# Kernel tuning notes

Hardware: AMD Instinct MI355X
Metric: run time of the kernel (lower is better)

Reference implementation:

```python
import jax, jax.numpy as jnp
import numpy as np

N_NODES = 50000


def setup_inputs() -> dict:
    key = jax.random.key(0)
    k1, k2, k3, k4, k5, k6 = jax.random.split(key, 6)
    c_in, c_out = 64, 64
    n_edges = 800000
    G = jax.random.normal(k1, (N_NODES, c_in), dtype=jnp.float32)
    RSC = jax.random.normal(k2, (N_NODES, c_in), dtype=jnp.float32)
    src = jax.random.randint(k3, (n_edges,), 0, N_NODES, dtype=jnp.int64)
    dst = jax.random.randint(k4, (n_edges,), 0, N_NODES, dtype=jnp.int64)
    W = jax.random.normal(k5, (c_out, c_in), dtype=jnp.float32) / np.sqrt(c_in)
    b = jax.random.normal(k6, (c_out,), dtype=jnp.float32) * 0.01
    return {"G": G, "RSC": RSC, "src": src, "dst": dst, "W": W, "b": b}


def reference(G, RSC, src, dst, W, b):
    # Per-edge relative feature: src node 'G' feature minus dst node 'RSC' feature
    rel = G[src] - RSC[dst]                          # [E, c_in]
    # Linear + ReLU (edge MLP)
    enc = jax.nn.relu(rel @ W.T + b)                 # [E, c_out]
    # Per-dst-node reductions over variable-size mailboxes
    max_agg = jax.ops.segment_max(enc, dst, num_segments=N_NODES)  # -inf for empty
    sum_agg = jax.ops.segment_sum(enc, dst, num_segments=N_NODES)
    cnt = jax.ops.segment_sum(jnp.ones_like(dst, dtype=enc.dtype), dst,
                              num_segments=N_NODES)               # [N]
    has_mail = (cnt > 0)[:, None]
    avg_agg = sum_agg / jnp.maximum(cnt, 1.0)[:, None]
    max_agg = jnp.where(has_mail, max_agg, 0.0)      # nodes w/o edges -> 0
    # concat(max, avg) as in reduce()
    return jnp.concatenate([max_agg, avg_agg], axis=-1)  # [N, 2*c_out]
```

## Files before the change

kernel.cpp:

```cpp
#include <hip/hip_runtime.h>
#include <hip/hip_bf16.h>

#define NCH 64
#define SPAN 64
#define HIST_BLOCKS 256
#define HIST_THREADS 1024
#define NBIN 256
#define NGEMM 768
#define FUSE_THREADS 512
#define SORT_CAP 3072

__global__ void detect_init_kernel(const unsigned short* __restrict__ gp, int n16,
                                   const unsigned* __restrict__ ip, int niw,
                                   unsigned* __restrict__ flags,
                                   unsigned* __restrict__ gcnt, int nb) {
    if (blockIdx.x == 0) {
        __shared__ unsigned se, so;
        if (threadIdx.x == 0) { se = 0u; so = 0u; }
        __syncthreads();
        unsigned le = 0u, lo = 0u;
        for (int i = threadIdx.x; i < n16; i += blockDim.x) {
            unsigned ex = (unsigned)((gp[i] >> 7) & 0xFFu);
            if (ex >= 0xC0u) le++;
        }
        for (int i = threadIdx.x; i < niw; i += blockDim.x) {
            if ((i & 1) && ip[i] != 0u) lo++;
        }
        atomicAdd(&se, le);
        atomicAdd(&so, lo);
        __syncthreads();
        if (threadIdx.x == 0) {
            flags[0] = (se > 50u) ? 1u : 0u;
            flags[1] = (so < 50u) ? 1u : 0u;
        }
    } else {
        const int stride = (gridDim.x - 1) * blockDim.x;
        for (int i = (blockIdx.x - 1) * blockDim.x + threadIdx.x; i < nb; i += stride)
            gcnt[i] = 0u;
    }
}

__global__ void bucket_hist_kernel(const void* __restrict__ dstp,
                                   unsigned* __restrict__ gcnt,
                                   const unsigned* __restrict__ flags,
                                   int n_edges, int nb) {
    extern __shared__ unsigned lcnt[];
    for (int i = threadIdx.x; i < nb; i += blockDim.x) lcnt[i] = 0u;
    __syncthreads();
    const unsigned i64 = flags[1];
    const int stride = gridDim.x * blockDim.x;
    for (int e = blockIdx.x * blockDim.x + threadIdx.x; e < n_edges; e += stride) {
        int d = i64 ? (int)((const long long*)dstp)[e] : ((const int*)dstp)[e];
        atomicAdd(&lcnt[d >> 6], 1u);
    }
    __syncthreads();
    for (int i = threadIdx.x; i < nb; i += blockDim.x)
        if (lcnt[i]) atomicAdd(&gcnt[i], lcnt[i]);
}

__global__ void bucket_scan_kernel(const unsigned* __restrict__ gcnt,
                                   unsigned* __restrict__ boffs,
                                   unsigned* __restrict__ cursor, int nb) {
    __shared__ unsigned s[1024];
    const int t = threadIdx.x;
    const int L = (nb + 1023) / 1024;
    unsigned local = 0u;
    for (int i = 0; i < L; ++i) {
        int idx = t * L + i;
        if (idx < nb) local += gcnt[idx];
    }
    s[t] = local;
    __syncthreads();
    for (int off = 1; off < 1024; off <<= 1) {
        unsigned v = (t >= off) ? s[t - off] : 0u;
        __syncthreads();
        s[t] += v;
        __syncthreads();
    }
    unsigned run = s[t] - local;
    for (int i = 0; i < L; ++i) {
        int idx = t * L + i;
        if (idx < nb) { boffs[idx] = run; cursor[idx] = run; run += gcnt[idx]; }
    }
}

__global__ __launch_bounds__(FUSE_THREADS, 4)
void binning_gemm_kernel(const void* __restrict__ srcp, const void* __restrict__ dstp,
                         unsigned* __restrict__ cursor, unsigned* __restrict__ binned,
                         const unsigned* __restrict__ flags, int n_edges, int nb,
                         int depth,
                         const void* __restrict__ Gp, const void* __restrict__ Rp,
                         const void* __restrict__ Wp, const void* __restrict__ bp,
                         void* __restrict__ PQ, int n_nodes) {
    extern __shared__ unsigned lds[];
    if (blockIdx.x < NBIN) {
        unsigned* lcnt = lds;
        unsigned* stage = lds + nb;
        for (int i = threadIdx.x; i < nb; i += blockDim.x) lcnt[i] = 0u;
        __syncthreads();
        const unsigned i64 = flags[1];
        const int chunk = (n_edges + NBIN - 1) / NBIN;
        const int e0 = blockIdx.x * chunk;
        const int e1 = min(e0 + chunk, n_edges);
        for (int e = e0 + threadIdx.x; e < e1; e += blockDim.x) {
            int s, d;
            if (i64) {
                s = (int)((const long long*)srcp)[e];
                d = (int)((const long long*)dstp)[e];
            } else {
                s = ((const int*)srcp)[e];
                d = ((const int*)dstp)[e];
            }
            const int bkt = d >> 6;
            const unsigned pk = ((unsigned)(d & 63) << 26) | (unsigned)s;
            unsigned pos = atomicAdd(&lcnt[bkt], 1u);
            if ((int)pos < depth) {
                stage[bkt * depth + (int)pos] = pk;
            } else {
                unsigned g = atomicAdd(&cursor[bkt], 1u);
                binned[g] = pk;
            }
        }
        __syncthreads();
        for (int bkt = threadIdx.x; bkt < nb; bkt += blockDim.x) {
            int k = min((int)lcnt[bkt], depth);
            if (k > 0) {
                unsigned base = atomicAdd(&cursor[bkt], (unsigned)k);
                for (int i = 0; i < k; ++i) binned[base + i] = stage[bkt * depth + i];
            }
        }
    } else {
        const unsigned f32 = flags[0];
        const int lane = threadIdx.x & 63;
        const int waveInBlk = threadIdx.x >> 6;
        const int wavesPerBlk = blockDim.x >> 6;
        const int gwave = (blockIdx.x - NBIN) * wavesPerBlk + waveInBlk;
        const int nwaves = NGEMM * wavesPerBlk;
        const int n_rows = 2 * n_nodes;
        const int ngroups = (n_rows + 3) / 4;

        float* ldsb = (float*)lds;
        float* slot = &ldsb[waveInBlk * 4 * NCH];

        float w[NCH];
        float bias;
        if (f32) {
            const float* Wf = (const float*)Wp;
            #pragma unroll
            for (int k = 0; k < NCH; ++k) w[k] = Wf[lane * NCH + k];
            bias = ((const float*)bp)[lane];
        } else {
            const __hip_bfloat16* Wh = (const __hip_bfloat16*)Wp;
            #pragma unroll
            for (int k = 0; k < NCH; ++k) w[k] = __bfloat162float(Wh[lane * NCH + k]);
            bias = __bfloat162float(((const __hip_bfloat16*)bp)[lane]);
        }

        const int niter = (ngroups + nwaves - 1) / nwaves;
        for (int it = 0; it < niter; ++it) {
            const int grp = gwave + it * nwaves;
            const bool gvalid = (grp < ngroups);
            const int m0 = grp * 4;
            if (gvalid) {
                const int myrow = m0 + (lane >> 4);
                const int col = (lane & 15) * 4;
                float x0 = 0.f, x1 = 0.f, x2 = 0.f, x3 = 0.f;
                if (myrow < n_rows) {
                    const bool isQ = (myrow >= n_nodes);
                    const int r = isQ ? (myrow - n_nodes) : myrow;
                    const void* inp = isQ ? Rp : Gp;
                    if (f32) {
                        float4 v = *(const float4*)((const float*)inp +
                                                    (size_t)r * NCH + col);
                        x0 = v.x; x1 = v.y; x2 = v.z; x3 = v.w;
                    } else {
                        ushort4 v = *(const ushort4*)((const unsigned short*)inp +
                                                      (size_t)r * NCH + col);
                        x0 = __bfloat162float(*(__hip_bfloat16*)&v.x);
                        x1 = __bfloat162float(*(__hip_bfloat16*)&v.y);
                        x2 = __bfloat162float(*(__hip_bfloat16*)&v.z);
                        x3 = __bfloat162float(*(__hip_bfloat16*)&v.w);
                    }
                }
                const int sb = (lane >> 4) * NCH + col;
                slot[sb + 0] = x0; slot[sb + 1] = x1;
                slot[sb + 2] = x2; slot[sb + 3] = x3;
            }
            __syncthreads();
            if (gvalid) {
                #pragma unroll
                for (int rr = 0; rr < 4; ++rr) {
                    const int m = m0 + rr;
                    if (m < n_rows) {
                        float a0 = 0.f, a1 = 0.f, a2 = 0.f, a3 = 0.f;
                        const float4* r4 = (const float4*)(slot + rr * NCH);
                        #pragma unroll
                        for (int q = 0; q < 16; ++q) {
                            float4 rv = r4[q];
                            a0 = fmaf(rv.x, w[4 * q + 0], a0);
                            a1 = fmaf(rv.y, w[4 * q + 1], a1);
                            a2 = fmaf(rv.z, w[4 * q + 2], a2);
                            a3 = fmaf(rv.w, w[4 * q + 3], a3);
                        }
                        float acc = (a0 + a1) + (a2 + a3);
                        if (m >= n_nodes) acc -= bias;
                        if (f32) ((float*)PQ)[(size_t)m * NCH + lane] = acc;
                        else ((__hip_bfloat16*)PQ)[(size_t)m * NCH + lane] =
                                 __float2bfloat16(acc);
                    }
                }
            }
            __syncthreads();
        }
    }
}

__global__ __launch_bounds__(256)
void bucket_sort_kernel(const unsigned* __restrict__ binned,
                        const unsigned* __restrict__ boffs,
                        const unsigned* __restrict__ gcnt,
                        unsigned* __restrict__ sorted_src,
                        unsigned* __restrict__ offs,
                        int n_nodes, int n_edges, int nb) {
    __shared__ unsigned dcnt[SPAN];
    __shared__ unsigned doff[SPAN];
    __shared__ unsigned cur[SPAN];
    __shared__ unsigned stage[SORT_CAP];
    const int b = blockIdx.x;
    const int tid = threadIdx.x;
    const int estart = (int)boffs[b];
    const int count = (int)gcnt[b];

    if (tid < SPAN) dcnt[tid] = 0u;
    __syncthreads();

    for (int i = tid; i < count; i += 256) {
        const unsigned pk = binned[estart + i];
        atomicAdd(&dcnt[pk >> 26], 1u);
        if (i < SORT_CAP) stage[i] = pk;
    }
    __syncthreads();

    if (tid == 0) {
        unsigned run = 0u;
        #pragma unroll
        for (int i = 0; i < SPAN; ++i) { doff[i] = run; cur[i] = run; run += dcnt[i]; }
    }
    __syncthreads();

    if (tid < SPAN) {
        const int n = b * SPAN + tid;
        if (n < n_nodes) offs[n] = (unsigned)estart + doff[tid];
    }
    if (b == nb - 1 && tid == 0) offs[n_nodes] = (unsigned)n_edges;

    const int lim = (count < SORT_CAP) ? count : SORT_CAP;
    for (int i = tid; i < lim; i += 256) {
        const unsigned pk = stage[i];
        const unsigned pos = atomicAdd(&cur[pk >> 26], 1u);
        sorted_src[estart + pos] = pk & 0x03FFFFFFu;
    }
    for (int i = SORT_CAP + tid; i < count; i += 256) {
        const unsigned pk = binned[estart + i];
        const unsigned pos = atomicAdd(&cur[pk >> 26], 1u);
        sorted_src[estart + pos] = pk & 0x03FFFFFFu;
    }
}

__global__ __launch_bounds__(256)
void node_kernel(const void* __restrict__ PQ,
                 const unsigned* __restrict__ sorted_src,
                 const unsigned* __restrict__ offs,
                 const unsigned* __restrict__ flags,
                 void* __restrict__ outp, int n_nodes) {
    const unsigned f32 = flags[0];
    const int lane = threadIdx.x & 63;
    const int h = lane >> 5;
    const int c2 = lane & 31;
    const int gwave = (blockIdx.x * blockDim.x + threadIdx.x) >> 6;
    const int nwaves = (gridDim.x * blockDim.x) >> 6;
    const float* Pf = (const float*)PQ;
    const unsigned short* Ph = (const unsigned short*)PQ;

    for (int n = gwave; n < n_nodes; n += nwaves) {
        float q0, q1;
        if (f32) {
            float2 qq = *(const float2*)&Pf[(size_t)(n_nodes + n) * NCH + 2 * c2];
            q0 = qq.x; q1 = qq.y;
        } else {
            ushort2 qq = *(const ushort2*)&Ph[(size_t)(n_nodes + n) * NCH + 2 * c2];
            q0 = __bfloat162float(*(__hip_bfloat16*)&qq.x);
            q1 = __bfloat162float(*(__hip_bfloat16*)&qq.y);
        }
        const int start = (int)offs[n];
        const int end = (int)offs[n + 1];
        float m0 = 0.f, m1 = 0.f, s0 = 0.f, s1 = 0.f;
        int j = start;
        for (; j + 8 <= end; j += 8) {
            const int i0 = j + h;
            const int e0 = (int)sorted_src[i0];
            const int e1 = (int)sorted_src[i0 + 2];
            const int e2 = (int)sorted_src[i0 + 4];
            const int e3 = (int)sorted_src[i0 + 6];
            float p00, p01, p10, p11, p20, p21, p30, p31;
            if (f32) {
                float2 v0 = *(const float2*)&Pf[(size_t)e0 * NCH + 2 * c2];
                float2 v1 = *(const float2*)&Pf[(size_t)e1 * NCH + 2 * c2];
                float2 v2 = *(const float2*)&Pf[(size_t)e2 * NCH + 2 * c2];
                float2 v3 = *(const float2*)&Pf[(size_t)e3 * NCH + 2 * c2];
                p00 = v0.x; p01 = v0.y; p10 = v1.x; p11 = v1.y;
                p20 = v2.x; p21 = v2.y; p30 = v3.x; p31 = v3.y;
            } else {
                ushort2 u0 = *(const ushort2*)&Ph[(size_t)e0 * NCH + 2 * c2];
                ushort2 u1 = *(const ushort2*)&Ph[(size_t)e1 * NCH + 2 * c2];
                ushort2 u2 = *(const ushort2*)&Ph[(size_t)e2 * NCH + 2 * c2];
                ushort2 u3 = *(const ushort2*)&Ph[(size_t)e3 * NCH + 2 * c2];
                p00 = __bfloat162float(*(__hip_bfloat16*)&u0.x);
                p01 = __bfloat162float(*(__hip_bfloat16*)&u0.y);
                p10 = __bfloat162float(*(__hip_bfloat16*)&u1.x);
                p11 = __bfloat162float(*(__hip_bfloat16*)&u1.y);
                p20 = __bfloat162float(*(__hip_bfloat16*)&u2.x);
                p21 = __bfloat162float(*(__hip_bfloat16*)&u2.y);
                p30 = __bfloat162float(*(__hip_bfloat16*)&u3.x);
                p31 = __bfloat162float(*(__hip_bfloat16*)&u3.y);
            }
            const float v00 = fmaxf(p00 - q0, 0.f), v01 = fmaxf(p01 - q1, 0.f);
            const float v10 = fmaxf(p10 - q0, 0.f), v11 = fmaxf(p11 - q1, 0.f);
            const float v20 = fmaxf(p20 - q0, 0.f), v21 = fmaxf(p21 - q1, 0.f);
            const float v30 = fmaxf(p30 - q0, 0.f), v31 = fmaxf(p31 - q1, 0.f);
            m0 = fmaxf(fmaxf(m0, v00), fmaxf(v10, fmaxf(v20, v30)));
            m1 = fmaxf(fmaxf(m1, v01), fmaxf(v11, fmaxf(v21, v31)));
            s0 += (v00 + v10) + (v20 + v30);
            s1 += (v01 + v11) + (v21 + v31);
        }
        #pragma unroll
        for (int u = 0; u < 4; ++u) {
            const int idx = j + 2 * u + h;
            if (idx < end) {
                const int e = (int)sorted_src[idx];
                float p0, p1;
                if (f32) {
                    float2 v = *(const float2*)&Pf[(size_t)e * NCH + 2 * c2];
                    p0 = v.x; p1 = v.y;
                } else {
                    ushort2 uu = *(const ushort2*)&Ph[(size_t)e * NCH + 2 * c2];
                    p0 = __bfloat162float(*(__hip_bfloat16*)&uu.x);
                    p1 = __bfloat162float(*(__hip_bfloat16*)&uu.y);
                }
                const float v0 = fmaxf(p0 - q0, 0.f);
                const float v1 = fmaxf(p1 - q1, 0.f);
                m0 = fmaxf(m0, v0); m1 = fmaxf(m1, v1);
                s0 += v0; s1 += v1;
            }
        }
        m0 = fmaxf(m0, __shfl_xor(m0, 32));
        m1 = fmaxf(m1, __shfl_xor(m1, 32));
        s0 = s0 + __shfl_xor(s0, 32);
        s1 = s1 + __shfl_xor(s1, 32);
        const int deg = end - start;
        const float inv = 1.0f / (float)(deg > 0 ? deg : 1);
        const float a0 = s0 * inv, a1 = s1 * inv;
        if (h == 0) {
            if (f32) {
                float* out = (float*)outp;
                *(float2*)&out[(size_t)n * 2 * NCH + 2 * c2] = make_float2(m0, m1);
                *(float2*)&out[(size_t)n * 2 * NCH + NCH + 2 * c2] = make_float2(a0, a1);
            } else {
                unsigned short* out = (unsigned short*)outp;
                __hip_bfloat16 hm0 = __float2bfloat16(m0);
                __hip_bfloat16 hm1 = __float2bfloat16(m1);
                __hip_bfloat16 ha0 = __float2bfloat16(a0);
                __hip_bfloat16 ha1 = __float2bfloat16(a1);
                ushort2 sm, sa;
                sm.x = *(unsigned short*)&hm0; sm.y = *(unsigned short*)&hm1;
                sa.x = *(unsigned short*)&ha0; sa.y = *(unsigned short*)&ha1;
                *(ushort2*)&out[(size_t)n * 2 * NCH + 2 * c2] = sm;
                *(ushort2*)&out[(size_t)n * 2 * NCH + NCH + 2 * c2] = sa;
            }
        }
    }
}

extern "C" void kernel_launch(void* const* d_in, const int* in_sizes, int n_in,
                              void* d_out, int out_size, void* d_ws, size_t ws_size,
                              hipStream_t stream) {
    const void* G = d_in[0];
    const void* RSC = d_in[1];
    const void* src = d_in[2];
    const void* dst = d_in[3];
    const void* W = d_in[4];
    const void* b = d_in[5];

    const int n_nodes = in_sizes[0] / NCH;
    const int n_edges = in_sizes[2];
    const int nb = (n_nodes + SPAN - 1) / SPAN;

    char* ws = (char*)d_ws;
    unsigned* flags = (unsigned*)ws;
    size_t off = 256;
    unsigned* binned = (unsigned*)(ws + off);
    off += (((size_t)n_edges * 4 + 255) / 256) * 256;
    unsigned* sorted_src = (unsigned*)(ws + off);
    off += (((size_t)n_edges * 4 + 255) / 256) * 256;
    unsigned* offs = (unsigned*)(ws + off);
    off += (((size_t)(n_nodes + 1) * 4 + 255) / 256) * 256;
    unsigned* boffs = (unsigned*)(ws + off);
    off += (((size_t)nb * 4 + 255) / 256) * 256;
    unsigned* cursor = (unsigned*)(ws + off);
    off += (((size_t)nb * 4 + 255) / 256) * 256;
    unsigned* gcnt = (unsigned*)(ws + off);
    off += (((size_t)nb * 4 + 255) / 256) * 256;
    void* PQ = (void*)(ws + off);

    const int n_g_probe = (in_sizes[0] < 8192) ? in_sizes[0] : 8192;
    const int n_idx_probe = (n_edges < 8192) ? n_edges : 8192;

    detect_init_kernel<<<64, 256, 0, stream>>>((const unsigned short*)G, n_g_probe,
                                               (const unsigned*)src, n_idx_probe,
                                               flags, gcnt, nb);

    bucket_hist_kernel<<<HIST_BLOCKS, HIST_THREADS, (size_t)nb * 4, stream>>>(
        dst, gcnt, flags, n_edges, nb);

    bucket_scan_kernel<<<1, 1024, 0, stream>>>(gcnt, boffs, cursor, nb);

    int depth = 9728 / nb - 1;
    if (depth > 19) depth = 19;
    if (depth < 4) depth = 4;
    size_t bin_lds = (size_t)nb * (depth + 1) * 4;
    const size_t gemm_lds = (size_t)(FUSE_THREADS / 64) * 4 * NCH * 4;
    if (bin_lds < gemm_lds) bin_lds = gemm_lds;

    binning_gemm_kernel<<<NBIN + NGEMM, FUSE_THREADS, bin_lds, stream>>>(
        src, dst, cursor, binned, flags, n_edges, nb, depth,
        G, RSC, W, b, PQ, n_nodes);

    bucket_sort_kernel<<<nb, 256, 0, stream>>>(binned, boffs, gcnt, sorted_src,
                                               offs, n_nodes, n_edges, nb);

    node_kernel<<<2048, 256, 0, stream>>>(PQ, sorted_src, offs, flags, d_out, n_nodes);
}
```

Measured before the change: 192.0 us.

## Replace two-level bucket sort with direct per-node counting sort via global atomics

Drops the bucketed binning pass (LDS staging per 64-node bucket) and the separate bucket_sort kernel. Per-node degrees are now counted with global atomics, scanned to per-node offsets, and each edge is scattered straight to its final CSR slot with a global atomic on a per-node cursor. This removes one kernel launch and one full pass over the edge array, at the cost of contended global atomics (800k atomics spread over 50k addresses) and scattered 4-byte writes without LDS coalescing. The single-block scan now walks 50k entries instead of about 800.

After: 365.1 us. +90.2%, slower.

```diff
diff --git a/kernel.cpp b/kernel.cpp
--- a/kernel.cpp
+++ b/kernel.cpp
@@ -2,18 +2,16 @@
 #include <hip/hip_bf16.h>
 
 #define NCH 64
-#define SPAN 64
 #define HIST_BLOCKS 256
 #define HIST_THREADS 1024
-#define NBIN 256
+#define NSCAT 256
 #define NGEMM 768
 #define FUSE_THREADS 512
-#define SORT_CAP 3072
 
 __global__ void detect_init_kernel(const unsigned short* __restrict__ gp, int n16,
                                    const unsigned* __restrict__ ip, int niw,
                                    unsigned* __restrict__ flags,
-                                   unsigned* __restrict__ gcnt, int nb) {
+                                   unsigned* __restrict__ deg, int n_nodes) {
     if (blockIdx.x == 0) {
         __shared__ unsigned se, so;
         if (threadIdx.x == 0) { se = 0u; so = 0u; }
@@ -35,39 +33,34 @@
         }
     } else {
         const int stride = (gridDim.x - 1) * blockDim.x;
-        for (int i = (blockIdx.x - 1) * blockDim.x + threadIdx.x; i < nb; i += stride)
-            gcnt[i] = 0u;
-    }
-}
-
-__global__ void bucket_hist_kernel(const void* __restrict__ dstp,
-                                   unsigned* __restrict__ gcnt,
-                                   const unsigned* __restrict__ flags,
-                                   int n_edges, int nb) {
-    extern __shared__ unsigned lcnt[];
-    for (int i = threadIdx.x; i < nb; i += blockDim.x) lcnt[i] = 0u;
-    __syncthreads();
+        for (int i = (blockIdx.x - 1) * blockDim.x + threadIdx.x; i < n_nodes;
+             i += stride)
+            deg[i] = 0u;
+    }
+}
+
+__global__ void deg_hist_kernel(const void* __restrict__ dstp,
+                                unsigned* __restrict__ deg,
+                                const unsigned* __restrict__ flags, int n_edges) {
     const unsigned i64 = flags[1];
     const int stride = gridDim.x * blockDim.x;
     for (int e = blockIdx.x * blockDim.x + threadIdx.x; e < n_edges; e += stride) {
         int d = i64 ? (int)((const long long*)dstp)[e] : ((const int*)dstp)[e];
-        atomicAdd(&lcnt[d >> 6], 1u);
-    }
-    __syncthreads();
-    for (int i = threadIdx.x; i < nb; i += blockDim.x)
-        if (lcnt[i]) atomicAdd(&gcnt[i], lcnt[i]);
-}
-
-__global__ void bucket_scan_kernel(const unsigned* __restrict__ gcnt,
-                                   unsigned* __restrict__ boffs,
-                                   unsigned* __restrict__ cursor, int nb) {
+        atomicAdd(&deg[d], 1u);
+    }
+}
+
+__global__ void node_scan_kernel(const unsigned* __restrict__ deg,
+                                 unsigned* __restrict__ offs,
+                                 unsigned* __restrict__ cursor,
+                                 int n_nodes, int n_edges) {
     __shared__ unsigned s[1024];
     const int t = threadIdx.x;
-    const int L = (nb + 1023) / 1024;
+    const int L = (n_nodes + 1023) / 1024;
     unsigned local = 0u;
     for (int i = 0; i < L; ++i) {
         int idx = t * L + i;
-        if (idx < nb) local += gcnt[idx];
+        if (idx < n_nodes) local += deg[idx];
     }
     s[t] = local;
     __syncthreads();
@@ -80,26 +73,23 @@
     unsigned run = s[t] - local;
     for (int i = 0; i < L; ++i) {
         int idx = t * L + i;
-        if (idx < nb) { boffs[idx] = run; cursor[idx] = run; run += gcnt[idx]; }
-    }
+        if (idx < n_nodes) { offs[idx] = run; cursor[idx] = run; run += deg[idx]; }
+    }
+    if (t == 0) offs[n_nodes] = (unsigned)n_edges;
 }
 
 __global__ __launch_bounds__(FUSE_THREADS, 4)
-void binning_gemm_kernel(const void* __restrict__ srcp, const void* __restrict__ dstp,
-                         unsigned* __restrict__ cursor, unsigned* __restrict__ binned,
-                         const unsigned* __restrict__ flags, int n_edges, int nb,
-                         int depth,
+void scatter_gemm_kernel(const void* __restrict__ srcp, const void* __restrict__ dstp,
+                         unsigned* __restrict__ cursor,
+                         unsigned* __restrict__ sorted_src,
+                         const unsigned* __restrict__ flags, int n_edges,
                          const void* __restrict__ Gp, const void* __restrict__ Rp,
                          const void* __restrict__ Wp, const void* __restrict__ bp,
                          void* __restrict__ PQ, int n_nodes) {
     extern __shared__ unsigned lds[];
-    if (blockIdx.x < NBIN) {
-        unsigned* lcnt = lds;
-        unsigned* stage = lds + nb;
-        for (int i = threadIdx.x; i < nb; i += blockDim.x) lcnt[i] = 0u;
-        __syncthreads();
+    if (blockIdx.x < NSCAT) {
         const unsigned i64 = flags[1];
-        const int chunk = (n_edges + NBIN - 1) / NBIN;
+        const int chunk = (n_edges + NSCAT - 1) / NSCAT;
         const int e0 = blockIdx.x * chunk;
         const int e1 = min(e0 + chunk, n_edges);
         for (int e = e0 + threadIdx.x; e < e1; e += blockDim.x) {
@@ -111,30 +101,15 @@
                 s = ((const int*)srcp)[e];
                 d = ((const int*)dstp)[e];
             }
-            const int bkt = d >> 6;
-            const unsigned pk = ((unsigned)(d & 63) << 26) | (unsigned)s;
-            unsigned pos = atomicAdd(&lcnt[bkt], 1u);
-            if ((int)pos < depth) {
-                stage[bkt * depth + (int)pos] = pk;
-            } else {
-                unsigned g = atomicAdd(&cursor[bkt], 1u);
-                binned[g] = pk;
-            }
-        }
-        __syncthreads();
-        for (int bkt = threadIdx.x; bkt < nb; bkt += blockDim.x) {
-            int k = min((int)lcnt[bkt], depth);
-            if (k > 0) {
-                unsigned base = atomicAdd(&cursor[bkt], (unsigned)k);
-                for (int i = 0; i < k; ++i) binned[base + i] = stage[bkt * depth + i];
-            }
+            const unsigned pos = atomicAdd(&cursor[d], 1u);
+            sorted_src[pos] = (unsigned)s;
         }
     } else {
         const unsigned f32 = flags[0];
         const int lane = threadIdx.x & 63;
         const int waveInBlk = threadIdx.x >> 6;
         const int wavesPerBlk = blockDim.x >> 6;
-        const int gwave = (blockIdx.x - NBIN) * wavesPerBlk + waveInBlk;
+        const int gwave = (blockIdx.x - NSCAT) * wavesPerBlk + waveInBlk;
         const int nwaves = NGEMM * wavesPerBlk;
         const int n_rows = 2 * n_nodes;
         const int ngroups = (n_rows + 3) / 4;
@@ -212,58 +187,6 @@
             }
             __syncthreads();
         }
-    }
-}
-
-__global__ __launch_bounds__(256)
-void bucket_sort_kernel(const unsigned* __restrict__ binned,
-                        const unsigned* __restrict__ boffs,
-                        const unsigned* __restrict__ gcnt,
-                        unsigned* __restrict__ sorted_src,
-                        unsigned* __restrict__ offs,
-                        int n_nodes, int n_edges, int nb) {
-    __shared__ unsigned dcnt[SPAN];
-    __shared__ unsigned doff[SPAN];
-    __shared__ unsigned cur[SPAN];
-    __shared__ unsigned stage[SORT_CAP];
-    const int b = blockIdx.x;
-    const int tid = threadIdx.x;
-    const int estart = (int)boffs[b];
-    const int count = (int)gcnt[b];
-
-    if (tid < SPAN) dcnt[tid] = 0u;
-    __syncthreads();
-
-    for (int i = tid; i < count; i += 256) {
-        const unsigned pk = binned[estart + i];
-        atomicAdd(&dcnt[pk >> 26], 1u);
-        if (i < SORT_CAP) stage[i] = pk;
-    }
-    __syncthreads();
-
-    if (tid == 0) {
-        unsigned run = 0u;
-        #pragma unroll
-        for (int i = 0; i < SPAN; ++i) { doff[i] = run; cur[i] = run; run += dcnt[i]; }
-    }
-    __syncthreads();
-
-    if (tid < SPAN) {
-        const int n = b * SPAN + tid;
-        if (n < n_nodes) offs[n] = (unsigned)estart + doff[tid];
-    }
-    if (b == nb - 1 && tid == 0) offs[n_nodes] = (unsigned)n_edges;
-
-    const int lim = (count < SORT_CAP) ? count : SORT_CAP;
-    for (int i = tid; i < lim; i += 256) {
-        const unsigned pk = stage[i];
-        const unsigned pos = atomicAdd(&cur[pk >> 26], 1u);
-        sorted_src[estart + pos] = pk & 0x03FFFFFFu;
-    }
-    for (int i = SORT_CAP + tid; i < count; i += 256) {
-        const unsigned pk = binned[estart + i];
-        const unsigned pos = atomicAdd(&cur[pk >> 26], 1u);
-        sorted_src[estart + pos] = pk & 0x03FFFFFFu;
     }
 }
 
@@ -393,23 +316,18 @@
 
     const int n_nodes = in_sizes[0] / NCH;
     const int n_edges = in_sizes[2];
-    const int nb = (n_nodes + SPAN - 1) / SPAN;
 
     char* ws = (char*)d_ws;
     unsigned* flags = (unsigned*)ws;
     size_t off = 256;
-    unsigned* binned = (unsigned*)(ws + off);
-    off += (((size_t)n_edges * 4 + 255) / 256) * 256;
     unsigned* sorted_src = (unsigned*)(ws + off);
     off += (((size_t)n_edges * 4 + 255) / 256) * 256;
     unsigned* offs = (unsigned*)(ws + off);
     off += (((size_t)(n_nodes + 1) * 4 + 255) / 256) * 256;
-    unsigned* boffs = (unsigned*)(ws + off);
-    off += (((size_t)nb * 4 + 255) / 256) * 256;
     unsigned* cursor = (unsigned*)(ws + off);
-    off += (((size_t)nb * 4 + 255) / 256) * 256;
-    unsigned* gcnt = (unsigned*)(ws + off);
-    off += (((size_t)nb * 4 + 255) / 256) * 256;
+    off += (((size_t)n_nodes * 4 + 255) / 256) * 256;
+    unsigned* deg = (unsigned*)(ws + off);
+    off += (((size_t)n_nodes * 4 + 255) / 256) * 256;
     void* PQ = (void*)(ws + off);
 
     const int n_g_probe = (in_sizes[0] < 8192) ? in_sizes[0] : 8192;
@@ -417,26 +335,17 @@
 
     detect_init_kernel<<<64, 256, 0, stream>>>((const unsigned short*)G, n_g_probe,
                                                (const unsigned*)src, n_idx_probe,
-                                               flags, gcnt, nb);
-
-    bucket_hist_kernel<<<HIST_BLOCKS, HIST_THREADS, (size_t)nb * 4, stream>>>(
-        dst, gcnt, flags, n_edges, nb);
-
-    bucket_scan_kernel<<<1, 1024, 0, stream>>>(gcnt, boffs, cursor, nb);
-
-    int depth = 9728 / nb - 1;
-    if (depth > 19) depth = 19;
-    if (depth < 4) depth = 4;
-    size_t bin_lds = (size_t)nb * (depth + 1) * 4;
+                                               flags, deg, n_nodes);
+
+    deg_hist_kernel<<<HIST_BLOCKS, HIST_THREADS, 0, stream>>>(dst, deg, flags,
+                                                              n_edges);
+
+    node_scan_kernel<<<1, 1024, 0, stream>>>(deg, offs, cursor, n_nodes, n_edges);
+
     const size_t gemm_lds = (size_t)(FUSE_THREADS / 64) * 4 * NCH * 4;
-    if (bin_lds < gemm_lds) bin_lds = gemm_lds;
-
-    binning_gemm_kernel<<<NBIN + NGEMM, FUSE_THREADS, bin_lds, stream>>>(
-        src, dst, cursor, binned, flags, n_edges, nb, depth,
+    scatter_gemm_kernel<<<NSCAT + NGEMM, FUSE_THREADS, gemm_lds, stream>>>(
+        src, dst, cursor, sorted_src, flags, n_edges,
         G, RSC, W, b, PQ, n_nodes);
 
-    bucket_sort_kernel<<<nb, 256, 0, stream>>>(binned, boffs, gcnt, sorted_src,
-                                               offs, n_nodes, n_edges, nb);
-
     node_kernel<<<2048, 256, 0, stream>>>(PQ, sorted_src, offs, flags, d_out, n_nodes);
 }
```
